# Performance work log

Hardware: AMD Instinct MI355X
Metric: run time of the kernel (lower is better)

Reference implementation:

```python
import jax, jax.numpy as jnp
import numpy as np

B, N, C = 2, 4096, 1024   # batch, input_size (seq), channels
H, Dh = 16, 64            # nhead, head_dim = channels // nhead
K = 256                   # dim_k (Linformer projected length)
FF = 4096                 # dim_ff
DEPTH = 2
EPS = 1e-5


def setup_inputs() -> dict:
    key = jax.random.key(0)
    ks = jax.random.split(key, 16)
    s = 0.02
    return {
        "x": jax.random.normal(ks[0], (B, N, C), jnp.float32),
        # per-layer, per-head Q/K/V projections: Linear(channels -> head_dim, bias=False)
        "Wq": jax.random.normal(ks[1], (DEPTH, H, C, Dh), jnp.float32) * s,
        "Wk": jax.random.normal(ks[2], (DEPTH, H, C, Dh), jnp.float32) * s,
        "Wv": jax.random.normal(ks[3], (DEPTH, H, C, Dh), jnp.float32) * s,
        # output proj: Linear(nhead*head_dim -> channels) with bias
        "Wo": jax.random.normal(ks[4], (DEPTH, H * Dh, C), jnp.float32) * s,
        "bo": jax.random.normal(ks[5], (DEPTH, C), jnp.float32) * s,
        # layerwise-shared E_proj = Linear(input_size -> dim_k) applied along seq axis
        # (same object used for both K and V projections)
        "Ew": jax.random.normal(ks[6], (K, N), jnp.float32) * (1.0 / np.sqrt(N)),
        "Eb": jax.random.normal(ks[7], (K,), jnp.float32) * s,
        # FeedForward: Linear(C->FF), gelu, Linear(FF->C)
        "W1": jax.random.normal(ks[8], (DEPTH, C, FF), jnp.float32) * s,
        "b1": jax.random.normal(ks[9], (DEPTH, FF), jnp.float32) * s,
        "W2": jax.random.normal(ks[10], (DEPTH, FF, C), jnp.float32) * s,
        "b2": jax.random.normal(ks[11], (DEPTH, C), jnp.float32) * s,
        # post-residual LayerNorm params: [layer, {attn, ff}, channels]
        "ln_g": 1.0 + 0.02 * jax.random.normal(ks[12], (DEPTH, 2, C), jnp.float32),
        "ln_b": 0.02 * jax.random.normal(ks[13], (DEPTH, 2, C), jnp.float32),
    }


def _layernorm(x, g, b):
    mu = jnp.mean(x, axis=-1, keepdims=True)
    var = jnp.var(x, axis=-1, keepdims=True)
    return (x - mu) * jax.lax.rsqrt(var + EPS) * g + b


def reference(x, Wq, Wk, Wv, Wo, bo, Ew, Eb, W1, b1, W2, b2, ln_g, ln_b):
    scale = 1.0 / np.sqrt(Dh)
    for l in range(DEPTH):
        # ---- Linformer multi-head attention (dropout = identity at inference) ----
        q = jnp.einsum('bnc,hcd->bhnd', x, Wq[l])   # [B,H,N,Dh]
        k = jnp.einsum('bnc,hcd->bhnd', x, Wk[l])
        v = jnp.einsum('bnc,hcd->bhnd', x, Wv[l])
        # project seq axis n -> k with shared E_proj (K^T @ E, V^T @ E)
        kp = jnp.einsum('bhnd,kn->bhkd', k, Ew) + Eb[None, None, :, None]  # [B,H,K,Dh]
        vp = jnp.einsum('bhnd,kn->bhkd', v, Ew) + Eb[None, None, :, None]
        p = jax.nn.softmax(jnp.einsum('bhnd,bhkd->bhnk', q, kp) * scale, axis=-1)
        o = jnp.einsum('bhnk,bhkd->bhnd', p, vp)
        o = o.transpose(0, 2, 1, 3).reshape(B, N, H * Dh)  # concat heads
        attn_out = o @ Wo[l] + bo[l]
        x = _layernorm(x + attn_out, ln_g[l, 0], ln_b[l, 0])  # Residual post-norm
        # ---- FeedForward ----
        h = jax.nn.gelu(x @ W1[l] + b1[l], approximate=False)
        ff_out = h @ W2[l] + b2[l]
        x = _layernorm(x + ff_out, ln_g[l, 1], ln_b[l, 1])
    return x
```

## Files before the change

### kernel.cpp

```cpp
#include <hip/hip_runtime.h>
#include <hip/hip_bf16.h>
#include <math.h>

typedef __bf16 bf16x8 __attribute__((ext_vector_type(8)));
typedef float f32x4 __attribute__((ext_vector_type(4)));

__global__ void cvt_f32_bf16(const float* __restrict__ in, __bf16* __restrict__ out, long n) {
    long i = ((long)blockIdx.x * 256 + threadIdx.x) * 4;
    long stride = (long)gridDim.x * 1024;
    for (; i < n; i += stride) {
        float4 v = *(const float4*)(in + i);
        out[i + 0] = (__bf16)v.x;
        out[i + 1] = (__bf16)v.y;
        out[i + 2] = (__bf16)v.z;
        out[i + 3] = (__bf16)v.w;
    }
}

__global__ void transpose_cvt(const float* __restrict__ in, __bf16* __restrict__ out,
                              int ldin, int ldout, long inBS, long outBS) {
    __shared__ __bf16 tile[32][33];
    in  += (long)blockIdx.z * inBS;
    out += (long)blockIdx.z * outBS;
    int n0 = blockIdx.x * 32, m0 = blockIdx.y * 32;
    for (int i = threadIdx.y; i < 32; i += 8)
        tile[i][threadIdx.x] = (__bf16)in[(long)(m0 + i) * ldin + n0 + threadIdx.x];
    __syncthreads();
    for (int i = threadIdx.y; i < 32; i += 8)
        out[(long)(n0 + i) * ldout + m0 + threadIdx.x] = tile[threadIdx.x][i];
}

__global__ void transpose_bf16(const __bf16* __restrict__ in, __bf16* __restrict__ out,
                               int rows, int cols) {
    __shared__ __bf16 tile[32][33];
    in  += (long)blockIdx.z * rows * cols;
    out += (long)blockIdx.z * rows * cols;
    int c0 = blockIdx.x * 32, r0 = blockIdx.y * 32;
    for (int i = threadIdx.y; i < 32; i += 8)
        tile[i][threadIdx.x] = in[(long)(r0 + i) * cols + c0 + threadIdx.x];
    __syncthreads();
    for (int i = threadIdx.y; i < 32; i += 8)
        out[(long)(c0 + i) * rows + r0 + threadIdx.x] = tile[threadIdx.x][i];
}

template<bool ROWB, bool COLB, bool GELUF, bool RES, int OUT>
__global__ __launch_bounds__(256, 2) void gemm_bf16(
    const __bf16* __restrict__ A, int lda, long aBS,
    const __bf16* __restrict__ Bt, int ldb, long bBS,
    void* __restrict__ outp, int ldc, long cBS,
    const float* __restrict__ rowBias,
    const float* __restrict__ colBias,
    const float* __restrict__ res, int ldres,
    int K)
{
    __shared__ __bf16 Asm[128 * 64];
    __shared__ __bf16 Bsm[128 * 64];
    const int tid = threadIdx.x;
    const int lane = tid & 63, wave = tid >> 6;
    const int wm = wave >> 1, wn = wave & 1;
    const int l15 = lane & 15, l4 = lane >> 4;

    int bx = blockIdx.x, by = blockIdx.y;
    {
        int gx = gridDim.x, gy = gridDim.y;
        int nb = gx * gy;
        if ((gx & 7) == 0 && (gy & 7) == 0 && (nb & 511) == 0) {
            int id = by * gx + bx;
            int xcd = id & 7, local = id >> 3;
            int t = local >> 6, within = local & 63;
            int ppx = gx >> 3;
            int ppc = nb >> 9;
            int pid = xcd * ppc + t;
            int pgy = pid / ppx, pgx = pid % ppx;
            bx = pgx * 8 + (within & 7);
            by = pgy * 8 + (within >> 3);
        } else if ((nb & 7) == 0) {
            int id = by * gx + bx;
            int cpx = nb >> 3;
            int swz = (id & 7) * cpx + (id >> 3);
            bx = swz % gx;
            by = swz / gx;
        }
    }
    const long m0 = (long)bx * 128, n0 = (long)by * 128;
    A  += (long)blockIdx.z * aBS;
    Bt += (long)blockIdx.z * bBS;

    const int srow8 = lane >> 3;
    const int gunit = ((lane & 7) ^ srow8) << 3;
    const __bf16* Abase = A  + (m0 + wave * 8 + srow8) * (long)lda + gunit;
    const __bf16* Bbase = Bt + (n0 + wave * 8 + srow8) * (long)ldb + gunit;
    __bf16* AsmW = Asm + wave * 8 * 64;
    __bf16* BsmW = Bsm + wave * 8 * 64;
    const int swz_r = l15 & 7;

    f32x4 acc[4][4];
#pragma unroll
    for (int mi = 0; mi < 4; mi++)
#pragma unroll
        for (int ni = 0; ni < 4; ni++) acc[mi][ni] = (f32x4){0.f, 0.f, 0.f, 0.f};

    for (int k0 = 0; k0 < K; k0 += 64) {
        __syncthreads();
#pragma unroll
        for (int p = 0; p < 4; p++) {
            __builtin_amdgcn_global_load_lds(
                (const __attribute__((address_space(1))) unsigned int*)(Abase + (long)p * 32 * lda + k0),
                (__attribute__((address_space(3))) unsigned int*)(AsmW + p * 32 * 64), 16, 0, 0);
            __builtin_amdgcn_global_load_lds(
                (const __attribute__((address_space(1))) unsigned int*)(Bbase + (long)p * 32 * ldb + k0),
                (__attribute__((address_space(3))) unsigned int*)(BsmW + p * 32 * 64), 16, 0, 0);
        }
        asm volatile("s_waitcnt vmcnt(0)" ::: "memory");
        __syncthreads();
#pragma unroll
        for (int ks = 0; ks < 2; ks++) {
            bf16x8 af[4], bfv[4];
#pragma unroll
            for (int mi = 0; mi < 4; mi++)
                af[mi] = *(const bf16x8*)(Asm + (wm * 64 + mi * 16 + l15) * 64 + (((ks * 4 + l4) ^ swz_r) << 3));
#pragma unroll
            for (int ni = 0; ni < 4; ni++)
                bfv[ni] = *(const bf16x8*)(Bsm + (wn * 64 + ni * 16 + l15) * 64 + (((ks * 4 + l4) ^ swz_r) << 3));
#pragma unroll
            for (int mi = 0; mi < 4; mi++)
#pragma unroll
                for (int ni = 0; ni < 4; ni++)
                    acc[mi][ni] = __builtin_amdgcn_mfma_f32_16x16x32_bf16(af[mi], bfv[ni], acc[mi][ni], 0, 0, 0);
        }
    }

    float* outf = (float*)outp;
    __bf16* outb = (__bf16*)outp;
    const long cOff = (long)blockIdx.z * cBS;
#pragma unroll
    for (int mi = 0; mi < 4; mi++)
#pragma unroll
        for (int ni = 0; ni < 4; ni++) {
            long gmb = m0 + wm * 64 + mi * 16 + l4 * 4;
            long gc  = n0 + wn * 64 + ni * 16 + l15;
#pragma unroll
            for (int i = 0; i < 4; i++) {
                long gm = gmb + i;
                float v = acc[mi][ni][i];
                if (ROWB)  v += rowBias[gm];
                if (COLB)  v += colBias[gc];
                if (GELUF) v = 0.5f * v * (1.f + erff(v * 0.70710678118f));
                if (RES)   v += res[gm * (long)ldres + gc];
                if (OUT == 0)      outf[cOff + gm * (long)ldc + gc] = v;
                else if (OUT == 1) outb[cOff + gm * (long)ldc + gc] = (__bf16)v;
                else               outb[cOff + gc * (long)ldc + gm] = (__bf16)v;
            }
        }
}

__global__ __launch_bounds__(256, 2) void gemm128_split(
    const __bf16* __restrict__ A, int lda, long aBS,
    const __bf16* __restrict__ Bt, int ldb, long bBS,
    float* __restrict__ P, long cBS, int ldc,
    int Ksplit, int S)
{
    __shared__ __bf16 Asm[128 * 64];
    __shared__ __bf16 Bsm[128 * 64];
    const int tid = threadIdx.x;
    const int lane = tid & 63, wave = tid >> 6;
    const int wm = wave >> 1, wn = wave & 1;
    const int l15 = lane & 15, l4 = lane >> 4;
    const long m0 = (long)blockIdx.x * 128, n0 = (long)blockIdx.y * 128;
    const long zb = blockIdx.z / S;
    const int  sp = blockIdx.z % S;
    A  += zb * aBS + (long)sp * Ksplit;
    Bt += zb * bBS + (long)sp * Ksplit;

    const int srow8 = lane >> 3;
    const int gunit = ((lane & 7) ^ srow8) << 3;
    const __bf16* Abase = A + (m0 + wave * 8 + srow8) * (long)lda + gunit;
    const __bf16* Bbase = Bt + (n0 + wave * 8 + srow8) * (long)ldb + gunit;
    __bf16* AsmW = Asm + wave * 8 * 64;
    __bf16* BsmW = Bsm + wave * 8 * 64;
    const int swz_r = l15 & 7;

    f32x4 acc[4][4];
#pragma unroll
    for (int mi = 0; mi < 4; mi++)
#pragma unroll
        for (int ni = 0; ni < 4; ni++) acc[mi][ni] = (f32x4){0.f, 0.f, 0.f, 0.f};

    for (int k0 = 0; k0 < Ksplit; k0 += 64) {
        __syncthreads();
#pragma unroll
        for (int p = 0; p < 4; p++) {
            __builtin_amdgcn_global_load_lds(
                (const __attribute__((address_space(1))) unsigned int*)(Abase + (long)p * 32 * lda + k0),
                (__attribute__((address_space(3))) unsigned int*)(AsmW + p * 32 * 64), 16, 0, 0);
            __builtin_amdgcn_global_load_lds(
                (const __attribute__((address_space(1))) unsigned int*)(Bbase + (long)p * 32 * ldb + k0),
                (__attribute__((address_space(3))) unsigned int*)(BsmW + p * 32 * 64), 16, 0, 0);
        }
        asm volatile("s_waitcnt vmcnt(0)" ::: "memory");
        __syncthreads();
#pragma unroll
        for (int ks = 0; ks < 2; ks++) {
            bf16x8 af[4], bfv[4];
#pragma unroll
            for (int mi = 0; mi < 4; mi++)
                af[mi] = *(const bf16x8*)(Asm + (wm * 64 + mi * 16 + l15) * 64 + (((ks * 4 + l4) ^ swz_r) << 3));
#pragma unroll
            for (int ni = 0; ni < 4; ni++)
                bfv[ni] = *(const bf16x8*)(Bsm + (wn * 64 + ni * 16 + l15) * 64 + (((ks * 4 + l4) ^ swz_r) << 3));
#pragma unroll
            for (int mi = 0; mi < 4; mi++)
#pragma unroll
                for (int ni = 0; ni < 4; ni++)
                    acc[mi][ni] = __builtin_amdgcn_mfma_f32_16x16x32_bf16(af[mi], bfv[ni], acc[mi][ni], 0, 0, 0);
        }
    }

    float* out = P + (long)blockIdx.z * cBS;
#pragma unroll
    for (int mi = 0; mi < 4; mi++)
#pragma unroll
        for (int ni = 0; ni < 4; ni++) {
            long gmb = m0 + wm * 64 + mi * 16 + l4 * 4;
            long gc  = n0 + wn * 64 + ni * 16 + l15;
#pragma unroll
            for (int i = 0; i < 4; i++)
                out[(gmb + i) * (long)ldc + gc] = acc[mi][ni][i];
        }
}

template<bool BIAS, bool TRANS>
__global__ __launch_bounds__(256) void reduce_partials(
    const float* __restrict__ P, __bf16* __restrict__ out,
    const float* __restrict__ bias, int S, int M, int N, long pBS)
{
    int b = blockIdx.z;
    long idx = ((long)blockIdx.x * 256 + threadIdx.x) * 4;
    if (idx >= (long)M * N) return;
    const float* Pb = P + (long)b * S * pBS + idx;
    float4 a = *(const float4*)Pb;
    for (int s = 1; s < S; s++) {
        float4 v = *(const float4*)(Pb + (long)s * pBS);
        a.x += v.x; a.y += v.y; a.z += v.z; a.w += v.w;
    }
    int m = (int)(idx / N), n = (int)(idx % N);
    if (BIAS) { float bv = bias[m]; a.x += bv; a.y += bv; a.z += bv; a.w += bv; }
    float av[4] = {a.x, a.y, a.z, a.w};
    if (!TRANS) {
        __bf16* o = out + (long)b * M * N + idx;
        o[0] = (__bf16)av[0]; o[1] = (__bf16)av[1]; o[2] = (__bf16)av[2]; o[3] = (__bf16)av[3];
    } else {
#pragma unroll
        for (int j = 0; j < 4; j++)
            out[(long)b * M * N + (long)(n + j) * M + m] = (__bf16)av[j];
    }
}

__global__ __launch_bounds__(256, 2) void attn_fused(
    const __bf16* __restrict__ Q, const __bf16* __restrict__ KP,
    const __bf16* __restrict__ VPt, __bf16* __restrict__ O)
{
    __shared__ __bf16 plds[4][4096];
    const int tid = threadIdx.x, lane = tid & 63, wave = tid >> 6;
    const int l15 = lane & 15, l4 = lane >> 4;
    const int h = blockIdx.y, b = blockIdx.z;
    const long row0 = (long)b * 4096 + (long)blockIdx.x * 64 + wave * 16;

    bf16x8 aq[2];
#pragma unroll
    for (int ks = 0; ks < 2; ks++)
        aq[ks] = *(const bf16x8*)(Q + (row0 + l15) * 1024 + h * 64 + ks * 32 + l4 * 8);

    f32x4 s[16];
#pragma unroll
    for (int f = 0; f < 16; f++) {
        f32x4 a = (f32x4){0.f, 0.f, 0.f, 0.f};
#pragma unroll
        for (int ks = 0; ks < 2; ks++) {
            bf16x8 bk = *(const bf16x8*)(KP + ((long)b * 256 + f * 16 + l15) * 1024 + h * 64 + ks * 32 + l4 * 8);
            a = __builtin_amdgcn_mfma_f32_16x16x32_bf16(aq[ks], bk, a, 0, 0, 0);
        }
        s[f] = a;
    }

    const float scale = 0.125f;
#pragma unroll
    for (int i = 0; i < 4; i++) {
        float m_ = -3.4e38f;
#pragma unroll
        for (int f = 0; f < 16; f++) { float v = s[f][i] * scale; s[f][i] = v; m_ = fmaxf(m_, v); }
#pragma unroll
        for (int msk = 1; msk < 16; msk <<= 1) m_ = fmaxf(m_, __shfl_xor(m_, msk));
        float su = 0.f;
#pragma unroll
        for (int f = 0; f < 16; f++) { float e = expf(s[f][i] - m_); s[f][i] = e; su += e; }
#pragma unroll
        for (int msk = 1; msk < 16; msk <<= 1) su += __shfl_xor(su, msk);
        float inv = 1.f / su;
#pragma unroll
        for (int f = 0; f < 16; f++) s[f][i] *= inv;
    }

    __bf16* pl = plds[wave];
#pragma unroll
    for (int f = 0; f < 16; f++)
#pragma unroll
        for (int i = 0; i < 4; i++) {
            int r = l4 * 4 + i, c = f * 16 + l15;
            int off = r * 256 + ((((c >> 3) ^ (r & 7)) << 3) | (c & 7));
            pl[off] = (__bf16)s[f][i];
        }

    f32x4 o[4];
#pragma unroll
    for (int f2 = 0; f2 < 4; f2++) o[f2] = (f32x4){0.f, 0.f, 0.f, 0.f};
#pragma unroll
    for (int ks = 0; ks < 8; ks++) {
        int kk = ks * 32 + l4 * 8;
        int off = l15 * 256 + (((kk >> 3) ^ (l15 & 7)) << 3);
        bf16x8 ap = *(const bf16x8*)(pl + off);
#pragma unroll
        for (int f2 = 0; f2 < 4; f2++) {
            bf16x8 bv = *(const bf16x8*)(VPt + ((long)b * 1024 + h * 64 + f2 * 16 + l15) * 256 + kk);
            o[f2] = __builtin_amdgcn_mfma_f32_16x16x32_bf16(ap, bv, o[f2], 0, 0, 0);
        }
    }
#pragma unroll
    for (int f2 = 0; f2 < 4; f2++)
#pragma unroll
        for (int i = 0; i < 4; i++)
            O[(row0 + l4 * 4 + i) * 1024 + h * 64 + f2 * 16 + l15] = (__bf16)o[f2][i];
}

__global__ __launch_bounds__(256) void ln_kernel(const float* __restrict__ y,
    const float* __restrict__ g, const float* __restrict__ b,
    float* __restrict__ xout, __bf16* __restrict__ xb)
{
    const int row = blockIdx.x;
    const int t = threadIdx.x;
    const float4 v = ((const float4*)(y + (long)row * 1024))[t];
    float s  = v.x + v.y + v.z + v.w;
    float ss = v.x * v.x + v.y * v.y + v.z * v.z + v.w * v.w;
#pragma unroll
    for (int m = 1; m < 64; m <<= 1) { s += __shfl_xor(s, m); ss += __shfl_xor(ss, m); }
    __shared__ float red[2][4];
    const int wave = t >> 6, lane = t & 63;
    if (lane == 0) { red[0][wave] = s; red[1][wave] = ss; }
    __syncthreads();
    s  = red[0][0] + red[0][1] + red[0][2] + red[0][3];
    ss = red[1][0] + red[1][1] + red[1][2] + red[1][3];
    const float mu = s * (1.f / 1024.f);
    const float var = ss * (1.f / 1024.f) - mu * mu;
    const float rs = rsqrtf(var + 1e-5f);
    const float4 gv = ((const float4*)g)[t];
    const float4 bv = ((const float4*)b)[t];
    float o0 = (v.x - mu) * rs * gv.x + bv.x;
    float o1 = (v.y - mu) * rs * gv.y + bv.y;
    float o2 = (v.z - mu) * rs * gv.z + bv.z;
    float o3 = (v.w - mu) * rs * gv.w + bv.w;
    float4 ov; ov.x = o0; ov.y = o1; ov.z = o2; ov.w = o3;
    ((float4*)(xout + (long)row * 1024))[t] = ov;
    __bf16* xr = xb + (long)row * 1024 + t * 4;
    xr[0] = (__bf16)o0; xr[1] = (__bf16)o1; xr[2] = (__bf16)o2; xr[3] = (__bf16)o3;
}

extern "C" void kernel_launch(void* const* d_in, const int* in_sizes, int n_in,
                              void* d_out, int out_size, void* d_ws, size_t ws_size,
                              hipStream_t stream) {
    const float* x   = (const float*)d_in[0];
    const float* Wq  = (const float*)d_in[1];
    const float* Wk  = (const float*)d_in[2];
    const float* Wv  = (const float*)d_in[3];
    const float* Wo  = (const float*)d_in[4];
    const float* bo  = (const float*)d_in[5];
    const float* Ew  = (const float*)d_in[6];
    const float* Eb  = (const float*)d_in[7];
    const float* W1  = (const float*)d_in[8];
    const float* b1  = (const float*)d_in[9];
    const float* W2  = (const float*)d_in[10];
    const float* b2  = (const float*)d_in[11];
    const float* lng = (const float*)d_in[12];
    const float* lnb = (const float*)d_in[13];
    float* xout = (float*)d_out;

    char* base = (char*)d_ws;
    size_t off = 0;
    auto alloc = [&](size_t bytes) { void* p = base + off; off += (bytes + 255) & ~(size_t)255; return p; };
    __bf16* Wqt = (__bf16*)alloc(2ll * 1024 * 1024 * 2);
    __bf16* Wkt = (__bf16*)alloc(2ll * 1024 * 1024 * 2);
    __bf16* Wvt = (__bf16*)alloc(2ll * 1024 * 1024 * 2);
    __bf16* Wot = (__bf16*)alloc(2ll * 1024 * 1024 * 2);
    __bf16* W1t = (__bf16*)alloc(2ll * 1024 * 4096 * 2);
    __bf16* W2t = (__bf16*)alloc(2ll * 1024 * 4096 * 2);
    __bf16* Ewb = (__bf16*)alloc(256ll * 4096 * 2);
    __bf16* xb  = (__bf16*)alloc(8192ll * 1024 * 2);
    __bf16* xbT = (__bf16*)alloc(2ll * 1024 * 4096 * 2);
    float*  y   = (float*) alloc(8192ll * 1024 * 4);
    __bf16* xp  = (__bf16*)alloc(2ll * 256 * 1024 * 2);
    __bf16* KPb = (__bf16*)alloc(2ll * 256 * 1024 * 2);
    __bf16* VPt = (__bf16*)alloc(2ll * 1024 * 256 * 2);
    __bf16* big = (__bf16*)alloc(8192ll * 4096 * 2);
    float*  xpP = (float*)big;
    float*  kpP = (float*)((char*)big + (16ll << 20));
    float*  vpP = (float*)((char*)big + (24ll << 20));
    __bf16* Qb  = big;
    __bf16* Ob  = big + (16ll << 20);
    __bf16* hbuf = big;

    cvt_f32_bf16<<<2048, 256, 0, stream>>>(x, xb, 8388608);
    cvt_f32_bf16<<<1024, 256, 0, stream>>>(Ew, Ewb, 1048576);
    transpose_cvt<<<dim3(2, 32, 32),  dim3(32, 8), 0, stream>>>(Wq, Wqt, 64, 1024, 65536, 65536);
    transpose_cvt<<<dim3(2, 32, 32),  dim3(32, 8), 0, stream>>>(Wk, Wkt, 64, 1024, 65536, 65536);
    transpose_cvt<<<dim3(2, 32, 32),  dim3(32, 8), 0, stream>>>(Wv, Wvt, 64, 1024, 65536, 65536);
    transpose_cvt<<<dim3(32, 32, 2),  dim3(32, 8), 0, stream>>>(Wo, Wot, 1024, 1024, 1048576, 1048576);
    transpose_cvt<<<dim3(128, 32, 2), dim3(32, 8), 0, stream>>>(W1, W1t, 4096, 1024, 4194304, 4194304);
    transpose_cvt<<<dim3(32, 128, 2), dim3(32, 8), 0, stream>>>(W2, W2t, 1024, 4096, 4194304, 4194304);

    for (int l = 0; l < 2; l++) {
        const __bf16* Wqt_l = Wqt + (long)l * 1048576;
        const __bf16* Wkt_l = Wkt + (long)l * 1048576;
        const __bf16* Wvt_l = Wvt + (long)l * 1048576;
        const __bf16* Wot_l = Wot + (long)l * 1048576;
        const __bf16* W1t_l = W1t + (long)l * 4194304;
        const __bf16* W2t_l = W2t + (long)l * 4194304;
        const float* res = (l == 0) ? x : xout;

        transpose_bf16<<<dim3(32, 128, 2), dim3(32, 8), 0, stream>>>(xb, xbT, 4096, 1024);
        gemm128_split<<<dim3(2, 8, 16), 256, 0, stream>>>(
            Ewb, 4096, 0, xbT, 4096, 4194304, xpP, 262144, 1024, 512, 8);
        reduce_partials<false, false><<<dim3(256, 1, 2), 256, 0, stream>>>(
            xpP, xp, nullptr, 8, 256, 1024, 262144);
        gemm128_split<<<dim3(2, 8, 8), 256, 0, stream>>>(
            xp, 1024, 262144, Wkt_l, 1024, 0, kpP, 262144, 1024, 256, 4);
        reduce_partials<true, false><<<dim3(256, 1, 2), 256, 0, stream>>>(
            kpP, KPb, Eb, 4, 256, 1024, 262144);
        gemm128_split<<<dim3(2, 8, 8), 256, 0, stream>>>(
            xp, 1024, 262144, Wvt_l, 1024, 0, vpP, 262144, 1024, 256, 4);
        reduce_partials<true, true><<<dim3(256, 1, 2), 256, 0, stream>>>(
            vpP, VPt, Eb, 4, 256, 1024, 262144);
        gemm_bf16<false, false, false, false, 1><<<dim3(64, 8, 1), 256, 0, stream>>>(
            xb, 1024, 0, Wqt_l, 1024, 0, (void*)Qb, 1024, 0, nullptr, nullptr, nullptr, 0, 1024);
        attn_fused<<<dim3(64, 16, 2), 256, 0, stream>>>(Qb, KPb, VPt, Ob);
        gemm_bf16<false, true, false, true, 0><<<dim3(64, 8, 1), 256, 0, stream>>>(
            Ob, 1024, 0, Wot_l, 1024, 0, (void*)y, 1024, 0,
            nullptr, bo + l * 1024, res, 1024, 1024);
        ln_kernel<<<8192, 256, 0, stream>>>(y, lng + (2 * l + 0) * 1024, lnb + (2 * l + 0) * 1024, xout, xb);
        gemm_bf16<false, true, true, false, 1><<<dim3(64, 32, 1), 256, 0, stream>>>(
            xb, 1024, 0, W1t_l, 1024, 0, (void*)hbuf, 4096, 0,
            nullptr, b1 + l * 4096, nullptr, 0, 1024);
        gemm_bf16<false, true, false, true, 0><<<dim3(64, 8, 1), 256, 0, stream>>>(
            hbuf, 4096, 0, W2t_l, 4096, 0, (void*)y, 1024, 0,
            nullptr, b2 + l * 1024, xout, 1024, 4096);
        ln_kernel<<<8192, 256, 0, stream>>>(y, lng + (2 * l + 1) * 1024, lnb + (2 * l + 1) * 1024, xout, xb);
    }
}
```

Baseline: 813.3 us.

## Merge K/V projection GEMMs and store pre-LayerNorm sums in bf16

Concatenates the transposed Wk and Wv weights so a single split-K GEMM computes both the K and V projections of the sequence-projected input. A new reduce_kv kernel writes K row-major and V transposed, adding the bias in the same pass. This replaces two GEMM launches and two reduce launches with one of each. Separately, the residual GEMM outputs feeding LayerNorm are now written as bf16 instead of fp32, halving that traffic at the cost of precision in the pre-norm sum.

```diff
diff --git a/kernel.cpp b/kernel.cpp
--- a/kernel.cpp
+++ b/kernel.cpp
@@ -3,6 +3,7 @@
 #include <math.h>
 
 typedef __bf16 bf16x8 __attribute__((ext_vector_type(8)));
+typedef __bf16 bf16x4 __attribute__((ext_vector_type(4)));
 typedef float f32x4 __attribute__((ext_vector_type(4)));
 
 __global__ void cvt_f32_bf16(const float* __restrict__ in, __bf16* __restrict__ out, long n) {
@@ -229,30 +230,45 @@
         }
 }
 
-template<bool BIAS, bool TRANS>
 __global__ __launch_bounds__(256) void reduce_partials(
-    const float* __restrict__ P, __bf16* __restrict__ out,
-    const float* __restrict__ bias, int S, int M, int N, long pBS)
+    const float* __restrict__ P, __bf16* __restrict__ out, int S, long total, long pBS)
 {
     int b = blockIdx.z;
     long idx = ((long)blockIdx.x * 256 + threadIdx.x) * 4;
-    if (idx >= (long)M * N) return;
+    if (idx >= total) return;
     const float* Pb = P + (long)b * S * pBS + idx;
     float4 a = *(const float4*)Pb;
     for (int s = 1; s < S; s++) {
         float4 v = *(const float4*)(Pb + (long)s * pBS);
         a.x += v.x; a.y += v.y; a.z += v.z; a.w += v.w;
     }
-    int m = (int)(idx / N), n = (int)(idx % N);
-    if (BIAS) { float bv = bias[m]; a.x += bv; a.y += bv; a.z += bv; a.w += bv; }
-    float av[4] = {a.x, a.y, a.z, a.w};
-    if (!TRANS) {
-        __bf16* o = out + (long)b * M * N + idx;
+    __bf16* o = out + (long)b * total + idx;
+    o[0] = (__bf16)a.x; o[1] = (__bf16)a.y; o[2] = (__bf16)a.z; o[3] = (__bf16)a.w;
+}
+
+__global__ __launch_bounds__(256) void reduce_kv(
+    const float* __restrict__ P, __bf16* __restrict__ KP, __bf16* __restrict__ VPt,
+    const float* __restrict__ Eb, int S)
+{
+    int b = blockIdx.z;
+    long idx = ((long)blockIdx.x * 256 + threadIdx.x) * 4;
+    const float* Pb = P + (long)b * S * 524288 + idx;
+    float4 a = *(const float4*)Pb;
+    for (int s = 1; s < S; s++) {
+        float4 v = *(const float4*)(Pb + (long)s * 524288);
+        a.x += v.x; a.y += v.y; a.z += v.z; a.w += v.w;
+    }
+    int m = (int)(idx >> 11), n = (int)(idx & 2047);
+    float bv = Eb[m];
+    float av[4] = {a.x + bv, a.y + bv, a.z + bv, a.w + bv};
+    if (n < 1024) {
+        __bf16* o = KP + (long)b * 262144 + (long)m * 1024 + n;
         o[0] = (__bf16)av[0]; o[1] = (__bf16)av[1]; o[2] = (__bf16)av[2]; o[3] = (__bf16)av[3];
     } else {
+        int c = n - 1024;
 #pragma unroll
         for (int j = 0; j < 4; j++)
-            out[(long)b * M * N + (long)(n + j) * M + m] = (__bf16)av[j];
+            VPt[(long)b * 262144 + (long)(c + j) * 256 + m] = (__bf16)av[j];
     }
 }
 
@@ -332,15 +348,16 @@
             O[(row0 + l4 * 4 + i) * 1024 + h * 64 + f2 * 16 + l15] = (__bf16)o[f2][i];
 }
 
-__global__ __launch_bounds__(256) void ln_kernel(const float* __restrict__ y,
+__global__ __launch_bounds__(256) void ln_kernel(const __bf16* __restrict__ y,
     const float* __restrict__ g, const float* __restrict__ b,
     float* __restrict__ xout, __bf16* __restrict__ xb)
 {
     const int row = blockIdx.x;
     const int t = threadIdx.x;
-    const float4 v = ((const float4*)(y + (long)row * 1024))[t];
-    float s  = v.x + v.y + v.z + v.w;
-    float ss = v.x * v.x + v.y * v.y + v.z * v.z + v.w * v.w;
+    bf16x4 yv = *(const bf16x4*)(y + (long)row * 1024 + t * 4);
+    float v0 = (float)yv[0], v1 = (float)yv[1], v2 = (float)yv[2], v3 = (float)yv[3];
+    float s  = v0 + v1 + v2 + v3;
+    float ss = v0 * v0 + v1 * v1 + v2 * v2 + v3 * v3;
 #pragma unroll
     for (int m = 1; m < 64; m <<= 1) { s += __shfl_xor(s, m); ss += __shfl_xor(ss, m); }
     __shared__ float red[2][4];
@@ -354,10 +371,10 @@
     const float rs = rsqrtf(var + 1e-5f);
     const float4 gv = ((const float4*)g)[t];
     const float4 bv = ((const float4*)b)[t];
-    float o0 = (v.x - mu) * rs * gv.x + bv.x;
-    float o1 = (v.y - mu) * rs * gv.y + bv.y;
-    float o2 = (v.z - mu) * rs * gv.z + bv.z;
-    float o3 = (v.w - mu) * rs * gv.w + bv.w;
+    float o0 = (v0 - mu) * rs * gv.x + bv.x;
+    float o1 = (v1 - mu) * rs * gv.y + bv.y;
+    float o2 = (v2 - mu) * rs * gv.z + bv.z;
+    float o3 = (v3 - mu) * rs * gv.w + bv.w;
     float4 ov; ov.x = o0; ov.y = o1; ov.z = o2; ov.w = o3;
     ((float4*)(xout + (long)row * 1024))[t] = ov;
     __bf16* xr = xb + (long)row * 1024 + t * 4;
@@ -386,71 +403,64 @@
     char* base = (char*)d_ws;
     size_t off = 0;
     auto alloc = [&](size_t bytes) { void* p = base + off; off += (bytes + 255) & ~(size_t)255; return p; };
-    __bf16* Wqt = (__bf16*)alloc(2ll * 1024 * 1024 * 2);
-    __bf16* Wkt = (__bf16*)alloc(2ll * 1024 * 1024 * 2);
-    __bf16* Wvt = (__bf16*)alloc(2ll * 1024 * 1024 * 2);
-    __bf16* Wot = (__bf16*)alloc(2ll * 1024 * 1024 * 2);
-    __bf16* W1t = (__bf16*)alloc(2ll * 1024 * 4096 * 2);
-    __bf16* W2t = (__bf16*)alloc(2ll * 1024 * 4096 * 2);
-    __bf16* Ewb = (__bf16*)alloc(256ll * 4096 * 2);
-    __bf16* xb  = (__bf16*)alloc(8192ll * 1024 * 2);
-    __bf16* xbT = (__bf16*)alloc(2ll * 1024 * 4096 * 2);
-    float*  y   = (float*) alloc(8192ll * 1024 * 4);
-    __bf16* xp  = (__bf16*)alloc(2ll * 256 * 1024 * 2);
-    __bf16* KPb = (__bf16*)alloc(2ll * 256 * 1024 * 2);
-    __bf16* VPt = (__bf16*)alloc(2ll * 1024 * 256 * 2);
-    __bf16* big = (__bf16*)alloc(8192ll * 4096 * 2);
-    float*  xpP = (float*)big;
-    float*  kpP = (float*)((char*)big + (16ll << 20));
-    float*  vpP = (float*)((char*)big + (24ll << 20));
-    __bf16* Qb  = big;
-    __bf16* Ob  = big + (16ll << 20);
+    __bf16* Wqt  = (__bf16*)alloc(2ll * 1024 * 1024 * 2);
+    __bf16* WkVt = (__bf16*)alloc(2ll * 2048 * 1024 * 2);
+    __bf16* Wot  = (__bf16*)alloc(2ll * 1024 * 1024 * 2);
+    __bf16* W1t  = (__bf16*)alloc(2ll * 1024 * 4096 * 2);
+    __bf16* W2t  = (__bf16*)alloc(2ll * 1024 * 4096 * 2);
+    __bf16* Ewb  = (__bf16*)alloc(256ll * 4096 * 2);
+    __bf16* xb   = (__bf16*)alloc(8192ll * 1024 * 2);
+    __bf16* xbT  = (__bf16*)alloc(2ll * 1024 * 4096 * 2);
+    __bf16* ybf  = (__bf16*)alloc(8192ll * 1024 * 2);
+    __bf16* xp   = (__bf16*)alloc(2ll * 256 * 1024 * 2);
+    __bf16* KPb  = (__bf16*)alloc(2ll * 256 * 1024 * 2);
+    __bf16* VPt  = (__bf16*)alloc(2ll * 1024 * 256 * 2);
+    __bf16* big  = (__bf16*)alloc(8192ll * 4096 * 2);
+    float*  xpP  = (float*)big;
+    float*  kvP  = (float*)((char*)big + (16ll << 20));
+    __bf16* Qb   = big;
+    __bf16* Ob   = big + (32ll << 20);
     __bf16* hbuf = big;
 
     cvt_f32_bf16<<<2048, 256, 0, stream>>>(x, xb, 8388608);
     cvt_f32_bf16<<<1024, 256, 0, stream>>>(Ew, Ewb, 1048576);
     transpose_cvt<<<dim3(2, 32, 32),  dim3(32, 8), 0, stream>>>(Wq, Wqt, 64, 1024, 65536, 65536);
-    transpose_cvt<<<dim3(2, 32, 32),  dim3(32, 8), 0, stream>>>(Wk, Wkt, 64, 1024, 65536, 65536);
-    transpose_cvt<<<dim3(2, 32, 32),  dim3(32, 8), 0, stream>>>(Wv, Wvt, 64, 1024, 65536, 65536);
+    transpose_cvt<<<dim3(2, 32, 16),  dim3(32, 8), 0, stream>>>(Wk,           WkVt,                     64, 1024, 65536, 65536);
+    transpose_cvt<<<dim3(2, 32, 16),  dim3(32, 8), 0, stream>>>(Wk + 1048576, WkVt + 2097152,           64, 1024, 65536, 65536);
+    transpose_cvt<<<dim3(2, 32, 16),  dim3(32, 8), 0, stream>>>(Wv,           WkVt + 1048576,           64, 1024, 65536, 65536);
+    transpose_cvt<<<dim3(2, 32, 16),  dim3(32, 8), 0, stream>>>(Wv + 1048576, WkVt + 2097152 + 1048576, 64, 1024, 65536, 65536);
     transpose_cvt<<<dim3(32, 32, 2),  dim3(32, 8), 0, stream>>>(Wo, Wot, 1024, 1024, 1048576, 1048576);
     transpose_cvt<<<dim3(128, 32, 2), dim3(32, 8), 0, stream>>>(W1, W1t, 4096, 1024, 4194304, 4194304);
     transpose_cvt<<<dim3(32, 128, 2), dim3(32, 8), 0, stream>>>(W2, W2t, 1024, 4096, 4194304, 4194304);
 
     for (int l = 0; l < 2; l++) {
-        const __bf16* Wqt_l = Wqt + (long)l * 1048576;
-        const __bf16* Wkt_l = Wkt + (long)l * 1048576;
-        const __bf16* Wvt_l = Wvt + (long)l * 1048576;
-        const __bf16* Wot_l = Wot + (long)l * 1048576;
-        const __bf16* W1t_l = W1t + (long)l * 4194304;
-        const __bf16* W2t_l = W2t + (long)l * 4194304;
+        const __bf16* Wqt_l  = Wqt  + (long)l * 1048576;
+        const __bf16* WkVt_l = WkVt + (long)l * 2097152;
+        const __bf16* Wot_l  = Wot  + (long)l * 1048576;
+        const __bf16* W1t_l  = W1t  + (long)l * 4194304;
+        const __bf16* W2t_l  = W2t  + (long)l * 4194304;
         const float* res = (l == 0) ? x : xout;
 
         transpose_bf16<<<dim3(32, 128, 2), dim3(32, 8), 0, stream>>>(xb, xbT, 4096, 1024);
         gemm128_split<<<dim3(2, 8, 16), 256, 0, stream>>>(
             Ewb, 4096, 0, xbT, 4096, 4194304, xpP, 262144, 1024, 512, 8);
-        reduce_partials<false, false><<<dim3(256, 1, 2), 256, 0, stream>>>(
-            xpP, xp, nullptr, 8, 256, 1024, 262144);
-        gemm128_split<<<dim3(2, 8, 8), 256, 0, stream>>>(
-            xp, 1024, 262144, Wkt_l, 1024, 0, kpP, 262144, 1024, 256, 4);
-        reduce_partials<true, false><<<dim3(256, 1, 2), 256, 0, stream>>>(
-            kpP, KPb, Eb, 4, 256, 1024, 262144);
-        gemm128_split<<<dim3(2, 8, 8), 256, 0, stream>>>(
-            xp, 1024, 262144, Wvt_l, 1024, 0, vpP, 262144, 1024, 256, 4);
-        reduce_partials<true, true><<<dim3(256, 1, 2), 256, 0, stream>>>(
-            vpP, VPt, Eb, 4, 256, 1024, 262144);
+        reduce_partials<<<dim3(256, 1, 2), 256, 0, stream>>>(xpP, xp, 8, 262144, 262144);
+        gemm128_split<<<dim3(2, 16, 8), 256, 0, stream>>>(
+            xp, 1024, 262144, WkVt_l, 1024, 0, kvP, 524288, 2048, 256, 4);
+        reduce_kv<<<dim3(512, 1, 2), 256, 0, stream>>>(kvP, KPb, VPt, Eb, 4);
         gemm_bf16<false, false, false, false, 1><<<dim3(64, 8, 1), 256, 0, stream>>>(
             xb, 1024, 0, Wqt_l, 1024, 0, (void*)Qb, 1024, 0, nullptr, nullptr, nullptr, 0, 1024);
         attn_fused<<<dim3(64, 16, 2), 256, 0, stream>>>(Qb, KPb, VPt, Ob);
-        gemm_bf16<false, true, false, true, 0><<<dim3(64, 8, 1), 256, 0, stream>>>(
-            Ob, 1024, 0, Wot_l, 1024, 0, (void*)y, 1024, 0,
+        gemm_bf16<false, true, false, true, 1><<<dim3(64, 8, 1), 256, 0, stream>>>(
+            Ob, 1024, 0, Wot_l, 1024, 0, (void*)ybf, 1024, 0,
             nullptr, bo + l * 1024, res, 1024, 1024);
-        ln_kernel<<<8192, 256, 0, stream>>>(y, lng + (2 * l + 0) * 1024, lnb + (2 * l + 0) * 1024, xout, xb);
+        ln_kernel<<<8192, 256, 0, stream>>>(ybf, lng + (2 * l + 0) * 1024, lnb + (2 * l + 0) * 1024, xout, xb);
         gemm_bf16<false, true, true, false, 1><<<dim3(64, 32, 1), 256, 0, stream>>>(
             xb, 1024, 0, W1t_l, 1024, 0, (void*)hbuf, 4096, 0,
             nullptr, b1 + l * 4096, nullptr, 0, 1024);
-        gemm_bf16<false, true, false, true, 0><<<dim3(64, 8, 1), 256, 0, stream>>>(
-            hbuf, 4096, 0, W2t_l, 4096, 0, (void*)y, 1024, 0,
+        gemm_bf16<false, true, false, true, 1><<<dim3(64, 8, 1), 256, 0, stream>>>(
+            hbuf, 4096, 0, W2t_l, 4096, 0, (void*)ybf, 1024, 0,
             nullptr, b2 + l * 1024, xout, 1024, 4096);
-        ln_kernel<<<8192, 256, 0, stream>>>(y, lng + (2 * l + 1) * 1024, lnb + (2 * l + 1) * 1024, xout, xb);
-    }
-}
+        ln_kernel<<<8192, 256, 0, stream>>>(ybf, lng + (2 * l + 1) * 1024, lnb + (2 * l + 1) * 1024, xout, xb);
+    }
+}
```

Result: no change. 808.4 us (-0.6%).
